# Performance work log

Measured on AMD Instinct MI355X. Metric: run time of the kernel, lower is better.

The kernel has to match this reference:

```python
import jax, jax.numpy as jnp
import numpy as np

D, H, C, T, B = 1024, 128, 256, 16, 8192


def setup_inputs() -> dict:
    key = jax.random.key(0)
    ks = jax.random.split(key, 7)
    s = 0.02
    return {
        "x": jax.random.normal(ks[0], (B, D), dtype=jnp.float32),
        "Wr": jax.random.normal(ks[1], (D, T), dtype=jnp.float32) * s,  # router weight (transposed vs torch)
        "br": jnp.zeros((T,), dtype=jnp.float32),
        "W1": jax.random.normal(ks[2], (T, D, H), dtype=jnp.float32) * s,  # per-task fc1
        "b1": jnp.zeros((T, H), dtype=jnp.float32),
        "W2": jax.random.normal(ks[3], (T, H, C), dtype=jnp.float32) * s,  # per-task fc2
        "b2": jnp.zeros((T, C), dtype=jnp.float32),
    }


def reference(x, Wr, br, W1, b1, W2, b2):
    # Router: softmax over tasks, [B, T]
    task_probs = jax.nn.softmax(x @ Wr + br, axis=1)
    # All task experts as one batched grouped-GEMM pass.
    h = jax.nn.relu(jnp.einsum("bd,tdh->tbh", x, W1) + b1[:, None, :])  # [T, B, H]
    preds = jnp.einsum("tbh,thc->tbc", h, W2) + b2[:, None, :]           # [T, B, C]
    # Weight each task's predictions by its routing probability.
    task_preds = preds * task_probs.T[:, :, None]                         # [T, B, C]
    return task_probs, task_preds
```

## Files before the change

kernel.cpp:

```cpp
#include <hip/hip_runtime.h>

using bf16x8 = __attribute__((ext_vector_type(8))) short;
using f32x4  = __attribute__((ext_vector_type(4))) float;

#define B_SZ 8192
#define D_SZ 1024
#define H_SZ 128
#define C_SZ 256
#define T_SZ 16

#define SB __builtin_amdgcn_sched_barrier(0)

__device__ __forceinline__ unsigned short f2bf(float f) {
  unsigned int u = __float_as_uint(f);
  return (unsigned short)((u + 0x7fffu + ((u >> 16) & 1u)) >> 16);
}

__global__ __launch_bounds__(256) void transpose_cast_kernel(const float* __restrict__ src,
                                                             unsigned short* __restrict__ dst,
                                                             int R, int C, int cshift) {
  __shared__ float tile[32][257];
  const int t = blockIdx.y;
  const int r0 = blockIdx.x * 32;
  const float* s = src + ((size_t)t * R + r0) * C;
  const int n = 32 * C;
  for (int idx = threadIdx.x; idx < n; idx += 256)
    tile[idx >> cshift][idx & (C - 1)] = s[idx];
  __syncthreads();
  unsigned short* d = dst + (size_t)t * C * R + r0;
  for (int idx = threadIdx.x; idx < n; idx += 256) {
    int cc = idx >> 5, rr = idx & 31;
    d[(size_t)cc * R + rr] = f2bf(tile[rr][cc]);
  }
}

__global__ __launch_bounds__(256) void router_cast_kernel(const float* __restrict__ x,
                                                          const float* __restrict__ Wr,
                                                          const float* __restrict__ br,
                                                          float* __restrict__ out0,
                                                          unsigned short* __restrict__ xb) {
  const int lane = threadIdx.x & 63;
  const int wid  = threadIdx.x >> 6;
  const int brow = blockIdx.x * 16 + wid * 4;
  float acc[4][16];
#pragma unroll
  for (int r = 0; r < 4; ++r)
#pragma unroll
    for (int tt = 0; tt < 16; ++tt) acc[r][tt] = 0.f;

#pragma unroll
  for (int it = 0; it < 4; ++it) {
    const int d0 = it * 256 + lane * 4;
    float wv[4][16];
#pragma unroll
    for (int dd = 0; dd < 4; ++dd) {
      const float4* w4 = (const float4*)(Wr + (size_t)(d0 + dd) * 16);
      float4 a = w4[0], b = w4[1], c = w4[2], d = w4[3];
      wv[dd][0]=a.x; wv[dd][1]=a.y; wv[dd][2]=a.z; wv[dd][3]=a.w;
      wv[dd][4]=b.x; wv[dd][5]=b.y; wv[dd][6]=b.z; wv[dd][7]=b.w;
      wv[dd][8]=c.x; wv[dd][9]=c.y; wv[dd][10]=c.z; wv[dd][11]=c.w;
      wv[dd][12]=d.x; wv[dd][13]=d.y; wv[dd][14]=d.z; wv[dd][15]=d.w;
    }
#pragma unroll
    for (int r = 0; r < 4; ++r) {
      const float4 xv = *(const float4*)(x + (size_t)(brow + r) * 1024 + d0);
      ushort4 o4;
      o4.x = f2bf(xv.x); o4.y = f2bf(xv.y); o4.z = f2bf(xv.z); o4.w = f2bf(xv.w);
      *(ushort4*)(xb + (size_t)(brow + r) * 1024 + d0) = o4;
      const float xs[4] = {xv.x, xv.y, xv.z, xv.w};
#pragma unroll
      for (int dd = 0; dd < 4; ++dd)
#pragma unroll
        for (int tt = 0; tt < 16; ++tt) acc[r][tt] += xs[dd] * wv[dd][tt];
    }
  }
#pragma unroll
  for (int off = 32; off >= 1; off >>= 1) {
#pragma unroll
    for (int r = 0; r < 4; ++r)
#pragma unroll
      for (int tt = 0; tt < 16; ++tt) acc[r][tt] += __shfl_xor(acc[r][tt], off);
  }
  if (lane == 0) {
#pragma unroll
    for (int r = 0; r < 4; ++r) {
      float v[16]; float m = -1e30f;
#pragma unroll
      for (int tt = 0; tt < 16; ++tt) { v[tt] = acc[r][tt] + br[tt]; m = fmaxf(m, v[tt]); }
      float ssum = 0.f;
#pragma unroll
      for (int tt = 0; tt < 16; ++tt) { v[tt] = __expf(v[tt] - m); ssum += v[tt]; }
      const float inv = 1.0f / ssum;
      float4* o = (float4*)(out0 + (size_t)(brow + r) * 16);
      o[0] = make_float4(v[0] * inv, v[1] * inv, v[2] * inv, v[3] * inv);
      o[1] = make_float4(v[4] * inv, v[5] * inv, v[6] * inv, v[7] * inv);
      o[2] = make_float4(v[8] * inv, v[9] * inv, v[10] * inv, v[11] * inv);
      o[3] = make_float4(v[12] * inv, v[13] * inv, v[14] * inv, v[15] * inv);
    }
  }
}

#define SW_OFF 32768

__global__ __launch_bounds__(256, 2) void expert_kernel(
    const unsigned short* __restrict__ xb, const unsigned short* __restrict__ w1b,
    const unsigned short* __restrict__ w2b, const float* __restrict__ b1,
    const float* __restrict__ b2, const float* __restrict__ probs,
    float* __restrict__ out1) {
  __shared__ __align__(16) char smem[65536];
  const int tid  = threadIdx.x;
  const int lane = tid & 63;
  const int w    = tid >> 6;
  const int l16  = lane & 15;
  const int l4   = lane >> 4;

  const int bid = blockIdx.x;
  const int lid = (bid & 7) * 128 + (bid >> 3);
  const int t   = lid & 15;
  const int b0  = (lid >> 4) * 128;

  const unsigned short* gp[8];
  unsigned int ldo[8];
#pragma unroll
  for (int it = 0; it < 8; ++it) {
    const unsigned int o = (unsigned int)w * 4096u + (unsigned int)(it & 3) * 1024u + (unsigned int)lane * 16u;
    const int row = (int)(o >> 7);
    const int cb  = (int)((o & 127u) ^ (((unsigned)row & 7u) << 4));
    gp[it]  = (it < 4) ? (xb + (size_t)(b0 + row) * 1024 + (cb >> 1))
                       : (w1b + (size_t)(t * 128 + row) * 1024 + (cb >> 1));
    ldo[it] = o;
  }

#define STAGE(curbuf, kt)                                                              \
  {                                                                                    \
    _Pragma("unroll")                                                                  \
    for (int it = 0; it < 8; ++it) {                                                   \
      const unsigned short* g = gp[it] + (kt) * 64;                                    \
      char* dd = smem + (it < 4 ? (curbuf) * 16384 + (int)ldo[it]                      \
                                : SW_OFF + (curbuf) * 16384 + (int)ldo[it]);           \
      __builtin_amdgcn_global_load_lds(                                                \
          (const __attribute__((address_space(1))) unsigned int*)g,                    \
          (__attribute__((address_space(3))) unsigned int*)dd, 16, 0, 0);              \
    }                                                                                  \
  }

  const int wn = w & 1;
  const int wm = w >> 1;
  f32x4 acc1[4][4] = {};

#define FC1_PHASE(curbuf, ks)                                                          \
  {                                                                                    \
    const int bx_base = (curbuf) * 16384;                                              \
    const int aw_base = SW_OFF + (curbuf) * 16384;                                     \
    const int cb = (ks) * 64 + l4 * 16;                                                \
    bf16x8 aw[4], bx[4];                                                               \
    _Pragma("unroll")                                                                  \
    for (int ni = 0; ni < 4; ++ni) {                                                   \
      const int row = wn * 64 + ni * 16 + l16;                                         \
      aw[ni] = *(const bf16x8*)(smem + aw_base + (row << 7) + (cb ^ ((row & 7) << 4)));\
    }                                                                                  \
    _Pragma("unroll")                                                                  \
    for (int mi = 0; mi < 4; ++mi) {                                                   \
      const int row = wm * 64 + mi * 16 + l16;                                         \
      bx[mi] = *(const bf16x8*)(smem + bx_base + (row << 7) + (cb ^ ((row & 7) << 4)));\
    }                                                                                  \
    __builtin_amdgcn_s_setprio(1);                                                     \
    _Pragma("unroll")                                                                  \
    for (int ni = 0; ni < 4; ++ni)                                                     \
      _Pragma("unroll")                                                                \
      for (int mi = 0; mi < 4; ++mi)                                                   \
        acc1[ni][mi] = __builtin_amdgcn_mfma_f32_16x16x32_bf16(aw[ni], bx[mi], acc1[ni][mi], 0, 0, 0); \
    __builtin_amdgcn_s_setprio(0);                                                     \
  }

  STAGE(0, 0);
  STAGE(1, 1);
  asm volatile("s_waitcnt vmcnt(8)" ::: "memory");
  SB; __builtin_amdgcn_s_barrier(); SB;

#pragma unroll
  for (int kt = 0; kt < 14; ++kt) {
    const int cur = kt & 1;
    FC1_PHASE(cur, 0);
    FC1_PHASE(cur, 1);
    SB; __builtin_amdgcn_s_barrier(); SB;
    STAGE(cur, kt + 2);
    asm volatile("s_waitcnt vmcnt(8)" ::: "memory");
    SB; __builtin_amdgcn_s_barrier(); SB;
  }
  FC1_PHASE(0, 0);
  FC1_PHASE(0, 1);
  SB; __builtin_amdgcn_s_barrier(); SB;
  asm volatile("s_waitcnt vmcnt(0)" ::: "memory");
  SB; __builtin_amdgcn_s_barrier(); SB;
  FC1_PHASE(1, 0);
  FC1_PHASE(1, 1);
  SB; __builtin_amdgcn_s_barrier(); SB;

#pragma unroll
  for (int ni = 0; ni < 4; ++ni) {
    const int n0 = wn * 64 + ni * 16 + l4 * 4;
    float bb[4];
#pragma unroll
    for (int r = 0; r < 4; ++r) bb[r] = b1[t * 128 + n0 + r];
#pragma unroll
    for (int mi = 0; mi < 4; ++mi) {
      const int m = wm * 64 + mi * 16 + l16;
      unsigned int pk[2];
#pragma unroll
      for (int h = 0; h < 2; ++h) {
        float v0 = fmaxf(acc1[ni][mi][2 * h + 0] + bb[2 * h + 0], 0.f);
        float v1 = fmaxf(acc1[ni][mi][2 * h + 1] + bb[2 * h + 1], 0.f);
        pk[h] = (unsigned int)f2bf(v0) | ((unsigned int)f2bf(v1) << 16);
      }
      const int byte = (m << 8) + ((n0 * 2) ^ ((m & 7) << 4));
      *(uint2*)(smem + byte) = make_uint2(pk[0], pk[1]);
    }
  }
  asm volatile("s_waitcnt lgkmcnt(0)" ::: "memory");
  SB; __builtin_amdgcn_s_barrier(); SB;

  const int wm2 = w >> 1;
  const int wc  = w & 1;
  f32x4 acc2[4][8] = {};
  const unsigned short* w2t = w2b + (size_t)t * C_SZ * H_SZ;

#pragma unroll
  for (int ks = 0; ks < 4; ++ks) {
    const int cb = ks * 64 + l4 * 16;
    bf16x8 ah[4];
#pragma unroll
    for (int mi = 0; mi < 4; ++mi) {
      const int row = wm2 * 64 + mi * 16 + l16;
      ah[mi] = *(const bf16x8*)(smem + (row << 8) + (cb ^ ((row & 7) << 4)));
    }
#pragma unroll
    for (int ci = 0; ci < 8; ++ci) {
      const int c = wc * 128 + ci * 16 + l16;
      bf16x8 bw = *(const bf16x8*)(w2t + (size_t)c * 128 + ks * 32 + l4 * 8);
#pragma unroll
      for (int mi = 0; mi < 4; ++mi)
        acc2[mi][ci] = __builtin_amdgcn_mfma_f32_16x16x32_bf16(ah[mi], bw, acc2[mi][ci], 0, 0, 0);
    }
  }

  const size_t outbase = (size_t)t * (size_t)(B_SZ * C_SZ);
#pragma unroll
  for (int mi = 0; mi < 4; ++mi) {
    const int m0 = wm2 * 64 + mi * 16 + l4 * 4;
    float pv[4];
#pragma unroll
    for (int r = 0; r < 4; ++r) pv[r] = probs[(size_t)(b0 + m0 + r) * 16 + t];
#pragma unroll
    for (int ci = 0; ci < 8; ++ci) {
      const int c = wc * 128 + ci * 16 + l16;
      const float bias = b2[t * 256 + c];
#pragma unroll
      for (int r = 0; r < 4; ++r)
        out1[outbase + (size_t)(b0 + m0 + r) * 256 + c] = (acc2[mi][ci][r] + bias) * pv[r];
    }
  }
}

extern "C" void kernel_launch(void* const* d_in, const int* in_sizes, int n_in,
                              void* d_out, int out_size, void* d_ws, size_t ws_size,
                              hipStream_t stream) {
  const float* x  = (const float*)d_in[0];
  const float* Wr = (const float*)d_in[1];
  const float* br = (const float*)d_in[2];
  const float* W1 = (const float*)d_in[3];
  const float* b1 = (const float*)d_in[4];
  const float* W2 = (const float*)d_in[5];
  const float* b2 = (const float*)d_in[6];
  float* out0 = (float*)d_out;
  float* out1 = out0 + (size_t)B_SZ * T_SZ;

  char* ws = (char*)d_ws;
  unsigned short* xb  = (unsigned short*)ws;
  unsigned short* w1b = (unsigned short*)(ws + (size_t)16777216);
  unsigned short* w2b = (unsigned short*)(ws + (size_t)16777216 + 4194304);

  router_cast_kernel<<<B_SZ / 16, 256, 0, stream>>>(x, Wr, br, out0, xb);
  transpose_cast_kernel<<<dim3(D_SZ / 32, T_SZ), 256, 0, stream>>>(W1, w1b, D_SZ, H_SZ, 7);
  transpose_cast_kernel<<<dim3(H_SZ / 32, T_SZ), 256, 0, stream>>>(W2, w2b, H_SZ, C_SZ, 8);
  expert_kernel<<<1024, 256, 0, stream>>>(xb, w1b, w2b, b1, b2, out0, out1);
}
```

Measured before the change: 109.2 us.

## Read full LDS tile into registers before barrier, overlap MFMAs with next stage load

The FC1 main loop now reads both k-halves of the current LDS buffer into registers, waits on LDS, and passes the barrier. It then issues the global-to-LDS prefetch for tile kt+2 into the same buffer before running the 32 MFMAs. Previously the MFMAs had to finish before the barrier that allowed the overwrite. The goal is to overlap the async global loads with matrix compute, at the cost of double the register footprint for A/B fragments, which may raise register pressure.

```diff
diff --git a/kernel.cpp b/kernel.cpp
--- a/kernel.cpp
+++ b/kernel.cpp
@@ -147,29 +147,38 @@
   const int wn = w & 1;
   const int wm = w >> 1;
   f32x4 acc1[4][4] = {};
-
-#define FC1_PHASE(curbuf, ks)                                                          \
+  bf16x8 aw[2][4], bx[2][4];
+
+#define READ16(curbuf)                                                                 \
   {                                                                                    \
     const int bx_base = (curbuf) * 16384;                                              \
     const int aw_base = SW_OFF + (curbuf) * 16384;                                     \
-    const int cb = (ks) * 64 + l4 * 16;                                                \
-    bf16x8 aw[4], bx[4];                                                               \
     _Pragma("unroll")                                                                  \
-    for (int ni = 0; ni < 4; ++ni) {                                                   \
-      const int row = wn * 64 + ni * 16 + l16;                                         \
-      aw[ni] = *(const bf16x8*)(smem + aw_base + (row << 7) + (cb ^ ((row & 7) << 4)));\
+    for (int ks = 0; ks < 2; ++ks) {                                                   \
+      const int cb = ks * 64 + l4 * 16;                                                \
+      _Pragma("unroll")                                                                \
+      for (int ni = 0; ni < 4; ++ni) {                                                 \
+        const int row = wn * 64 + ni * 16 + l16;                                       \
+        aw[ks][ni] = *(const bf16x8*)(smem + aw_base + (row << 7) + (cb ^ ((row & 7) << 4))); \
+      }                                                                                \
+      _Pragma("unroll")                                                                \
+      for (int mi = 0; mi < 4; ++mi) {                                                 \
+        const int row = wm * 64 + mi * 16 + l16;                                       \
+        bx[ks][mi] = *(const bf16x8*)(smem + bx_base + (row << 7) + (cb ^ ((row & 7) << 4))); \
+      }                                                                                \
     }                                                                                  \
-    _Pragma("unroll")                                                                  \
-    for (int mi = 0; mi < 4; ++mi) {                                                   \
-      const int row = wm * 64 + mi * 16 + l16;                                         \
-      bx[mi] = *(const bf16x8*)(smem + bx_base + (row << 7) + (cb ^ ((row & 7) << 4)));\
-    }                                                                                  \
+  }
+
+#define MFMA32                                                                         \
+  {                                                                                    \
     __builtin_amdgcn_s_setprio(1);                                                     \
     _Pragma("unroll")                                                                  \
-    for (int ni = 0; ni < 4; ++ni)                                                     \
+    for (int ks = 0; ks < 2; ++ks)                                                     \
       _Pragma("unroll")                                                                \
-      for (int mi = 0; mi < 4; ++mi)                                                   \
-        acc1[ni][mi] = __builtin_amdgcn_mfma_f32_16x16x32_bf16(aw[ni], bx[mi], acc1[ni][mi], 0, 0, 0); \
+      for (int ni = 0; ni < 4; ++ni)                                                   \
+        _Pragma("unroll")                                                              \
+        for (int mi = 0; mi < 4; ++mi)                                                 \
+          acc1[ni][mi] = __builtin_amdgcn_mfma_f32_16x16x32_bf16(aw[ks][ni], bx[ks][mi], acc1[ni][mi], 0, 0, 0); \
     __builtin_amdgcn_s_setprio(0);                                                     \
   }
 
@@ -181,21 +190,25 @@
 #pragma unroll
   for (int kt = 0; kt < 14; ++kt) {
     const int cur = kt & 1;
-    FC1_PHASE(cur, 0);
-    FC1_PHASE(cur, 1);
+    READ16(cur);
+    asm volatile("s_waitcnt lgkmcnt(0)" ::: "memory");
     SB; __builtin_amdgcn_s_barrier(); SB;
     STAGE(cur, kt + 2);
+    SB;
+    MFMA32;
     asm volatile("s_waitcnt vmcnt(8)" ::: "memory");
     SB; __builtin_amdgcn_s_barrier(); SB;
   }
-  FC1_PHASE(0, 0);
-  FC1_PHASE(0, 1);
-  SB; __builtin_amdgcn_s_barrier(); SB;
+  READ16(0);
+  asm volatile("s_waitcnt lgkmcnt(0)" ::: "memory");
+  SB; __builtin_amdgcn_s_barrier(); SB;
+  MFMA32;
   asm volatile("s_waitcnt vmcnt(0)" ::: "memory");
   SB; __builtin_amdgcn_s_barrier(); SB;
-  FC1_PHASE(1, 0);
-  FC1_PHASE(1, 1);
-  SB; __builtin_amdgcn_s_barrier(); SB;
+  READ16(1);
+  asm volatile("s_waitcnt lgkmcnt(0)" ::: "memory");
+  SB; __builtin_amdgcn_s_barrier(); SB;
+  MFMA32;
 
 #pragma unroll
   for (int ni = 0; ni < 4; ++ni) {
```

Measured after the change: 109.4 us. About the same (+0.2%).
